# Kernel optimization log

Measured on AMD Instinct MI355X. Metric: run time of the kernel, lower is better.

## Reference

```python
import jax, jax.numpy as jnp
import numpy as np

IMG_SIZE = 640.0
CONF_THRESH = 0.001
NMS_THRESH = 0.6
TOP_K = 1000  # fixed-shape candidate cap per class


def _pairwise_iou(b):
    # b: [K,4] in x1,y1,x2,y2; replicates the numpy NMS math (1e-28 / 1e-14 eps)
    x1, y1, x2, y2 = b[:, 0], b[:, 1], b[:, 2], b[:, 3]
    areas = (x2 - x1) * (y2 - y1)
    xx1 = jnp.maximum(x1[:, None], x1[None, :])
    yy1 = jnp.maximum(y1[:, None], y1[None, :])
    xx2 = jnp.minimum(x2[:, None], x2[None, :])
    yy2 = jnp.minimum(y2[:, None], y2[None, :])
    w = jnp.maximum(1e-28, xx2 - xx1)
    h = jnp.maximum(1e-28, yy2 - yy1)
    inter = w * h
    return inter / (areas[:, None] + areas[None, :] - inter + 1e-14)


def setup_inputs() -> dict:
    key = jax.random.key(0)
    k1, k2, k3 = jax.random.split(key, 3)
    img_size, strides, KA, C = 640, [8, 16, 32], 3, 80
    anchor = np.array([[10, 13], [16, 30], [33, 23], [30, 61], [62, 45], [59, 119],
                       [116, 90], [156, 198], [373, 326]], np.float32).reshape(3, 3, 2)
    grids, anchs, strs = [], [], []
    for lvl, s in enumerate(strides):
        f = img_size // s
        gy, gx = np.meshgrid(np.arange(f), np.arange(f), indexing='ij')
        gxy = np.stack([gx, gy], -1).reshape(-1, 1, 2).astype(np.float32)
        grids.append(np.broadcast_to(gxy, (f * f, KA, 2)).reshape(-1, 2))
        anchs.append(np.broadcast_to(anchor[lvl][None], (f * f, KA, 2)).reshape(-1, 2).astype(np.float32))
        strs.append(np.full((f * f * KA, 1), s, np.float32))
    grid_xy = jnp.asarray(np.concatenate(grids, 0))      # [N,2]
    anchors_wh = jnp.asarray(np.concatenate(anchs, 0))   # [N,2]
    stride_t = jnp.asarray(np.concatenate(strs, 0))      # [N,1]
    N = grid_xy.shape[0]  # 25200
    return {
        'reg_pred': jax.random.normal(k1, (N, 4), jnp.float32),
        'obj_pred': jax.random.normal(k2, (N, 1), jnp.float32),
        'cls_pred': jax.random.normal(k3, (N, C), jnp.float32),
        'grid_xy': grid_xy,
        'anchors_wh': anchors_wh,
        'stride_t': stride_t,
    }


def reference(reg_pred, obj_pred, cls_pred, grid_xy, anchors_wh, stride_t):
    # ---- box decode (YOLO head) ----
    xy = (jax.nn.sigmoid(reg_pred[:, :2]) + grid_xy) * stride_t       # centers in pixels
    wh = jnp.exp(reg_pred[:, 2:]) * anchors_wh                        # sizes in pixels
    boxes = jnp.concatenate([xy - 0.5 * wh, xy + 0.5 * wh], axis=-1)  # [N,4]
    boxes = jnp.clip(boxes / IMG_SIZE, 0.0, 1.0)
    # ---- scoring: sigmoid(obj) * softmax(cls) ----
    scores_all = jax.nn.sigmoid(obj_pred) * jax.nn.softmax(cls_pred, axis=-1)  # [N,C]
    cls_inds = jnp.argmax(scores_all, axis=-1)          # [N]
    scores = jnp.max(scores_all, axis=-1)               # [N]
    C = cls_pred.shape[-1]
    K = TOP_K
    ar = jnp.arange(K)

    def nms_class(c):
        s_c = jnp.where((cls_inds == c) & (scores >= CONF_THRESH), scores, -1.0)
        vals, idx = jax.lax.top_k(s_c, K)               # sorted desc, fixed shape
        b = boxes[idx]                                  # [K,4]
        valid = vals > 0.0
        iou = _pairwise_iou(b)                          # [K,K]

        def body(i, keep):
            sup = keep[i] & (iou[i] > NMS_THRESH) & (ar > i)
            return keep & ~sup

        keep = jax.lax.fori_loop(0, K, body, valid)
        return b, vals, keep

    boxes_out, scores_out, keep = jax.vmap(nms_class)(jnp.arange(C))  # [C,K,4],[C,K],[C,K]
    return boxes_out, scores_out * keep.astype(scores_out.dtype), keep
```

## Files before the change

kernel.cpp:

```cpp
#include <hip/hip_runtime.h>
#include <cstdint>
#include <cstddef>

#define N_CLS 80
#define TOPK 1000
#define POOL_N 2048
#define MCAP 512
#define BD 1024
#define DTB 128
#define NBLK 197
#define SLICE 32
#define LDSB_STRIDE 10

__global__ __launch_bounds__(DTB) void decode_kernel(
    const float* __restrict__ reg, const float* __restrict__ obj,
    const float* __restrict__ cls, const float* __restrict__ grid,
    const float* __restrict__ anch, const float* __restrict__ strd,
    float* __restrict__ boxes, uint2* __restrict__ scs,
    int* __restrict__ cnts, uint2* __restrict__ gpool2, int N) {
  __shared__ int hcnt[N_CLS];
  __shared__ uint2 lpool[N_CLS * SLICE];
  const int blk = blockIdx.x;
  const int tid = threadIdx.x;
  const int i = blk * DTB + tid;

  if (tid < N_CLS) hcnt[tid] = 0;
  __syncthreads();

  const bool valid = (i < N);
  float best = -1.0f;
  int bc = 0;

  if (valid) {
    const float4 r = ((const float4*)reg)[i];
    const float2 g = ((const float2*)grid)[i];
    const float2 aw = ((const float2*)anch)[i];
    const float st = strd[i];

    float cx = (1.0f / (1.0f + expf(-r.x)) + g.x) * st;
    float cy = (1.0f / (1.0f + expf(-r.y)) + g.y) * st;
    float w = expf(r.z) * aw.x;
    float h = expf(r.w) * aw.y;
    float b0 = fminf(fmaxf((cx - 0.5f * w) / 640.0f, 0.0f), 1.0f);
    float b1 = fminf(fmaxf((cy - 0.5f * h) / 640.0f, 0.0f), 1.0f);
    float b2 = fminf(fmaxf((cx + 0.5f * w) / 640.0f, 0.0f), 1.0f);
    float b3 = fminf(fmaxf((cy + 0.5f * h) / 640.0f, 0.0f), 1.0f);
    float4 bo; bo.x = b0; bo.y = b1; bo.z = b2; bo.w = b3;
    ((float4*)boxes)[i] = bo;

    const float4* cr = (const float4*)cls + (size_t)i * 20;

    float mx;
    {
      float4 v = cr[0];
      mx = v.x;
      mx = fmaxf(mx, v.y); mx = fmaxf(mx, v.z); mx = fmaxf(mx, v.w);
#pragma unroll
      for (int q = 1; q < 20; ++q) {
        float4 u = cr[q];
        mx = fmaxf(mx, u.x); mx = fmaxf(mx, u.y);
        mx = fmaxf(mx, u.z); mx = fmaxf(mx, u.w);
      }
    }
    asm volatile("" ::: "memory");

    float s = 0.0f;
#pragma unroll
    for (int q = 0; q < 20; ++q) {
      float4 u = cr[q];
      s += expf(u.x - mx); s += expf(u.y - mx);
      s += expf(u.z - mx); s += expf(u.w - mx);
    }
    asm volatile("" ::: "memory");

    float sig = 1.0f / (1.0f + expf(-obj[i]));

#pragma unroll
    for (int q = 0; q < 20; ++q) {
      float4 u = cr[q];
      float e0 = expf(u.x - mx), e1 = expf(u.y - mx);
      float e2 = expf(u.z - mx), e3 = expf(u.w - mx);
      float q0 = sig * (e0 / s);
      if (q0 > best) { best = q0; bc = 4 * q + 0; }
      float q1 = sig * (e1 / s);
      if (q1 > best) { best = q1; bc = 4 * q + 1; }
      float q2 = sig * (e2 / s);
      if (q2 > best) { best = q2; bc = 4 * q + 2; }
      float q3 = sig * (e3 / s);
      if (q3 > best) { best = q3; bc = 4 * q + 3; }
    }
    scs[i] = make_uint2(__float_as_uint(best), (unsigned)bc);
  }

  const bool pos = valid && (best >= 0.001f);
  if (pos) {
    int slot = atomicAdd(&hcnt[bc], 1);
    if (slot < SLICE)
      lpool[bc * SLICE + slot] = make_uint2(__float_as_uint(best), (unsigned)i);
  }
  __syncthreads();
  if (tid < N_CLS) cnts[blk * N_CLS + tid] = min(hcnt[tid], SLICE);
  for (int t = tid; t < N_CLS * SLICE; t += DTB) {
    int c = t / SLICE, sl = t - c * SLICE;
    gpool2[((size_t)c * NBLK + blk) * SLICE + sl] = lpool[t];
  }
}

__device__ __forceinline__ unsigned long long kinit(int w, int m) {
  int lo = w << 6;
  return (m <= lo) ? 0ULL : ((m - lo >= 64) ? ~0ULL : ((1ULL << (m - lo)) - 1ULL));
}

__global__ __launch_bounds__(BD) void nms_kernel(
    const float* __restrict__ boxes, const uint2* __restrict__ scs,
    const int* __restrict__ cnts, const uint2* __restrict__ gpool2,
    float* __restrict__ out, int N) {
  const int c = blockIdx.x;
  const int tid = threadIdx.x;

  __shared__ uint2 pool[POOL_N];
  __shared__ float svals[TOPK];
  __shared__ int sidx[TOPK];
  __shared__ __align__(16) float4 bxyz[TOPK];
  __shared__ __align__(16) unsigned long long ldsB[MCAP * LDSB_STRIDE];
  __shared__ unsigned char kp[TOPK];
  __shared__ __align__(16) unsigned long long kmbuf[2][8];
  __shared__ int wsum[BD / 64 + 1];
  __shared__ int pref[NBLK + 1];

  if (tid < 64) {
    int carry = 0;
    if (tid == 0) pref[0] = 0;
    for (int ch = 0; ch < (NBLK + 63) / 64; ++ch) {
      int b = ch * 64 + tid;
      int v = (b < NBLK) ? cnts[b * N_CLS + c] : 0;
#pragma unroll
      for (int s = 1; s < 64; s <<= 1) {
        int u = __shfl_up(v, s, 64);
        if (tid >= (unsigned)s) v += u;
      }
      if (b < NBLK) pref[b + 1] = min(carry + v, POOL_N);
      carry += __shfl(v, 63, 64);
    }
  }
  __syncthreads();
  const int cnt = pref[NBLK];
  const int m = min(cnt, TOPK);

  const uint2* gp = gpool2 + (size_t)c * NBLK * SLICE;
  for (int t = tid; t < cnt; t += BD) {
    int lo = 0, hi = NBLK;
    while (hi - lo > 1) {
      int mid = (lo + hi) >> 1;
      if (t >= pref[mid]) lo = mid; else hi = mid;
    }
    pool[t] = gp[(size_t)lo * SLICE + (t - pref[lo])];
  }
  __syncthreads();

  for (int e = tid; e < cnt; e += BD) {
    uint2 me = pool[e];
    float v = __uint_as_float(me.x);
    int idx = (int)me.y;
    int r = 0;
#pragma unroll 8
    for (int k = 0; k < cnt; ++k) {
      uint2 q = pool[k];
      float vk = __uint_as_float(q.x);
      r += (int)((vk > v) || (vk == v && (int)q.y < idx));
    }
    if (r < TOPK) { svals[r] = v; sidx[r] = idx; }
  }
  __syncthreads();

  const int M = TOPK - m;
  if (M > 0) {
    int i = tid;
    bool f = false;
    if (i < N) {
      uint2 sc = scs[i];
      f = !((int)sc.y == c && __uint_as_float(sc.x) >= 0.001f);
    }
    unsigned long long mk = __ballot(f ? 1 : 0);
    int lane = tid & 63, wv = tid >> 6;
    int pre = __popcll(mk & ((1ULL << lane) - 1ULL));
    if (lane == 0) wsum[wv] = __popcll(mk);
    __syncthreads();
    if (tid == 0) {
      int acc = 0;
      for (int wq = 0; wq < BD / 64; ++wq) { int t2 = wsum[wq]; wsum[wq] = acc; acc += t2; }
    }
    __syncthreads();
    int pos = wsum[wv] + pre;
    if (f && pos < M) sidx[m + pos] = i;
  }
  __syncthreads();

  const float4* bf4 = (const float4*)boxes;
  for (int t = tid; t < TOPK; t += BD) bxyz[t] = bf4[sidx[t]];
  __syncthreads();

  const int W = (m + 63) >> 6;
  const bool fast = (m > 0) && (m <= MCAP);
  int cur = 0;

  if (fast) {
    const int tasks = m * W;
    for (int q = tid; q < tasks; q += BD) {
      int w = q / m;
      int j = q - w * m;
      unsigned long long bits = 0ULL;
      if (w <= (j >> 6)) {
        float4 jb = bxyz[j];
        float aj = (jb.z - jb.x) * (jb.w - jb.y);
        int i0 = w << 6, iend = min(i0 + 64, j);
        for (int i = i0; i < iend; ++i) {
          float4 ib = bxyz[i];
          float ai = (ib.z - ib.x) * (ib.w - ib.y);
          float xx1 = fmaxf(ib.x, jb.x), yy1 = fmaxf(ib.y, jb.y);
          float xx2 = fminf(ib.z, jb.z), yy2 = fminf(ib.w, jb.w);
          float ww = fmaxf(1e-28f, xx2 - xx1), hh = fmaxf(1e-28f, yy2 - yy1);
          float inter = ww * hh;
          float iou = inter / (ai + aj - inter + 1e-14f);
          if (iou > 0.6f) bits |= (1ULL << (i - i0));
        }
      }
      ldsB[(size_t)j * LDSB_STRIDE + w] = bits;
    }
    __syncthreads();

    ulonglong2 ta, tb, tc, td;
    ta = tb = tc = td = make_ulonglong2(0ULL, 0ULL);
    if (tid < m) {
      const ulonglong2* rp = (const ulonglong2*)&ldsB[(size_t)tid * LDSB_STRIDE];
      ta = rp[0]; tb = rp[1]; tc = rp[2]; td = rp[3];
    }
    if (tid < 8) kmbuf[0][tid] = kinit(tid, m);
    __syncthreads();

    for (;;) {
      bool keep = false;
      if (tid < m) {
        unsigned long long sup =
            (ta.x & kmbuf[cur][0]) | (ta.y & kmbuf[cur][1]) |
            (tb.x & kmbuf[cur][2]) | (tb.y & kmbuf[cur][3]) |
            (tc.x & kmbuf[cur][4]) | (tc.y & kmbuf[cur][5]) |
            (td.x & kmbuf[cur][6]) | (td.y & kmbuf[cur][7]);
        keep = (sup == 0ULL);
      }
      bool old = (tid < m) &&
                 ((kmbuf[cur][tid >> 6] >> (tid & 63)) & 1ULL);
      unsigned long long bl = __ballot(keep ? 1 : 0);
      int wv = tid >> 6;
      if ((tid & 63) == 0 && wv < 8) kmbuf[cur ^ 1][wv] = bl;
      int any = __syncthreads_or((int)(keep != old));
      cur ^= 1;
      if (!any) break;
    }
  } else {
    for (int t = tid; t < TOPK; t += BD) kp[t] = (t < m) ? 1 : 0;
    __syncthreads();
    for (int i = 0; i < m; ++i) {
      if (kp[i]) {
        float4 rb = bxyz[i];
        float ai = (rb.z - rb.x) * (rb.w - rb.y);
        for (int j = i + 1 + tid; j < m; j += BD) {
          if (kp[j]) {
            float4 jb = bxyz[j];
            float aj = (jb.z - jb.x) * (jb.w - jb.y);
            float xx1 = fmaxf(rb.x, jb.x), yy1 = fmaxf(rb.y, jb.y);
            float xx2 = fminf(rb.z, jb.z), yy2 = fminf(rb.w, jb.w);
            float ww = fmaxf(1e-28f, xx2 - xx1), hh = fmaxf(1e-28f, yy2 - yy1);
            float inter = ww * hh;
            float iou = inter / (ai + aj - inter + 1e-14f);
            if (iou > 0.6f) kp[j] = 0;
          }
        }
      }
      __syncthreads();
    }
  }

  float* outB = out;
  float* outS = out + N_CLS * TOPK * 4;
  float* outK = outS + N_CLS * TOPK;
  for (int t = tid; t < TOPK; t += BD) {
    float k = 0.0f;
    if (t < m)
      k = fast ? (float)((kmbuf[cur][t >> 6] >> (t & 63)) & 1ULL)
               : (float)kp[t];
    float v = (t < m) ? svals[t] : -1.0f;
    ((float4*)outB)[c * TOPK + t] = bxyz[t];
    outS[c * TOPK + t] = v * k;
    outK[c * TOPK + t] = k;
  }
}

extern "C" void kernel_launch(void* const* d_in, const int* in_sizes, int n_in,
                              void* d_out, int out_size, void* d_ws, size_t ws_size,
                              hipStream_t stream) {
  const float* reg  = (const float*)d_in[0];
  const float* obj  = (const float*)d_in[1];
  const float* cls  = (const float*)d_in[2];
  const float* grid = (const float*)d_in[3];
  const float* anch = (const float*)d_in[4];
  const float* strd = (const float*)d_in[5];
  const int N = in_sizes[0] / 4;

  char* w8 = (char*)d_ws;
  size_t off = 0;
  float* boxes  = (float*)(w8 + off); off += (size_t)N * 16;
  uint2* scs    = (uint2*)(w8 + off); off += (size_t)N * 8;
  int*   cnts   = (int*)(w8 + off);   off += (size_t)NBLK * N_CLS * 4;
  uint2* gpool2 = (uint2*)(w8 + off); off += (size_t)N_CLS * NBLK * SLICE * 8;
  float* out = (float*)d_out;

  decode_kernel<<<NBLK, DTB, 0, stream>>>(
      reg, obj, cls, grid, anch, strd, boxes, scs, cnts, gpool2, N);
  nms_kernel<<<N_CLS, BD, 0, stream>>>(boxes, scs, cnts, gpool2, out, N);
}
```

Baseline: 117.4 us.

## Decode boxes lazily in NMS kernel and drop full-size box/score buffers

```diff
diff --git a/kernel.cpp b/kernel.cpp
--- a/kernel.cpp
+++ b/kernel.cpp
@@ -13,13 +13,9 @@
 #define LDSB_STRIDE 10
 
 __global__ __launch_bounds__(DTB) void decode_kernel(
-    const float* __restrict__ reg, const float* __restrict__ obj,
-    const float* __restrict__ cls, const float* __restrict__ grid,
-    const float* __restrict__ anch, const float* __restrict__ strd,
-    float* __restrict__ boxes, uint2* __restrict__ scs,
+    const float* __restrict__ obj, const float* __restrict__ cls,
     int* __restrict__ cnts, uint2* __restrict__ gpool2, int N) {
   __shared__ int hcnt[N_CLS];
-  __shared__ uint2 lpool[N_CLS * SLICE];
   const int blk = blockIdx.x;
   const int tid = threadIdx.x;
   const int i = blk * DTB + tid;
@@ -32,22 +28,6 @@
   int bc = 0;
 
   if (valid) {
-    const float4 r = ((const float4*)reg)[i];
-    const float2 g = ((const float2*)grid)[i];
-    const float2 aw = ((const float2*)anch)[i];
-    const float st = strd[i];
-
-    float cx = (1.0f / (1.0f + expf(-r.x)) + g.x) * st;
-    float cy = (1.0f / (1.0f + expf(-r.y)) + g.y) * st;
-    float w = expf(r.z) * aw.x;
-    float h = expf(r.w) * aw.y;
-    float b0 = fminf(fmaxf((cx - 0.5f * w) / 640.0f, 0.0f), 1.0f);
-    float b1 = fminf(fmaxf((cy - 0.5f * h) / 640.0f, 0.0f), 1.0f);
-    float b2 = fminf(fmaxf((cx + 0.5f * w) / 640.0f, 0.0f), 1.0f);
-    float b3 = fminf(fmaxf((cy + 0.5f * h) / 640.0f, 0.0f), 1.0f);
-    float4 bo; bo.x = b0; bo.y = b1; bo.z = b2; bo.w = b3;
-    ((float4*)boxes)[i] = bo;
-
     const float4* cr = (const float4*)cls + (size_t)i * 20;
 
     float mx;
@@ -89,21 +69,16 @@
       float q3 = sig * (e3 / s);
       if (q3 > best) { best = q3; bc = 4 * q + 3; }
     }
-    scs[i] = make_uint2(__float_as_uint(best), (unsigned)bc);
   }
 
   const bool pos = valid && (best >= 0.001f);
-  if (pos) {
-    int slot = atomicAdd(&hcnt[bc], 1);
-    if (slot < SLICE)
-      lpool[bc * SLICE + slot] = make_uint2(__float_as_uint(best), (unsigned)i);
-  }
-  __syncthreads();
-  if (tid < N_CLS) cnts[blk * N_CLS + tid] = min(hcnt[tid], SLICE);
-  for (int t = tid; t < N_CLS * SLICE; t += DTB) {
-    int c = t / SLICE, sl = t - c * SLICE;
-    gpool2[((size_t)c * NBLK + blk) * SLICE + sl] = lpool[t];
-  }
+  int slot = -1;
+  if (pos) slot = atomicAdd(&hcnt[bc], 1);
+  __syncthreads();
+  if (tid < N_CLS) cnts[tid * NBLK + blk] = min(hcnt[tid], SLICE);
+  if (pos && slot < SLICE)
+    gpool2[((size_t)bc * NBLK + blk) * SLICE + slot] =
+        make_uint2(__float_as_uint(best), (unsigned)i);
 }
 
 __device__ __forceinline__ unsigned long long kinit(int w, int m) {
@@ -112,7 +87,8 @@
 }
 
 __global__ __launch_bounds__(BD) void nms_kernel(
-    const float* __restrict__ boxes, const uint2* __restrict__ scs,
+    const float* __restrict__ reg, const float* __restrict__ grid,
+    const float* __restrict__ anch, const float* __restrict__ strd,
     const int* __restrict__ cnts, const uint2* __restrict__ gpool2,
     float* __restrict__ out, int N) {
   const int c = blockIdx.x;
@@ -127,13 +103,15 @@
   __shared__ __align__(16) unsigned long long kmbuf[2][8];
   __shared__ int wsum[BD / 64 + 1];
   __shared__ int pref[NBLK + 1];
+  __shared__ unsigned fmap[32];
 
   if (tid < 64) {
+    const int* cc = cnts + c * NBLK;
     int carry = 0;
     if (tid == 0) pref[0] = 0;
     for (int ch = 0; ch < (NBLK + 63) / 64; ++ch) {
       int b = ch * 64 + tid;
-      int v = (b < NBLK) ? cnts[b * N_CLS + c] : 0;
+      int v = (b < NBLK) ? cc[b] : 0;
 #pragma unroll
       for (int s = 1; s < 64; s <<= 1) {
         int u = __shfl_up(v, s, 64);
@@ -143,6 +121,7 @@
       carry += __shfl(v, 63, 64);
     }
   }
+  if (tid < 32) fmap[tid] = 0u;
   __syncthreads();
   const int cnt = pref[NBLK];
   const int m = min(cnt, TOPK);
@@ -157,6 +136,11 @@
     pool[t] = gp[(size_t)lo * SLICE + (t - pref[lo])];
   }
   __syncthreads();
+
+  for (int t = tid; t < cnt; t += BD) {
+    unsigned idx = pool[t].y;
+    if (idx < 1024u) atomicOr(&fmap[idx >> 5], 1u << (idx & 31u));
+  }
 
   for (int e = tid; e < cnt; e += BD) {
     uint2 me = pool[e];
@@ -175,12 +159,7 @@
 
   const int M = TOPK - m;
   if (M > 0) {
-    int i = tid;
-    bool f = false;
-    if (i < N) {
-      uint2 sc = scs[i];
-      f = !((int)sc.y == c && __uint_as_float(sc.x) >= 0.001f);
-    }
+    bool f = !((fmap[tid >> 5] >> (tid & 31u)) & 1u);
     unsigned long long mk = __ballot(f ? 1 : 0);
     int lane = tid & 63, wv = tid >> 6;
     int pre = __popcll(mk & ((1ULL << lane) - 1ULL));
@@ -192,12 +171,27 @@
     }
     __syncthreads();
     int pos = wsum[wv] + pre;
-    if (f && pos < M) sidx[m + pos] = i;
-  }
-  __syncthreads();
-
-  const float4* bf4 = (const float4*)boxes;
-  for (int t = tid; t < TOPK; t += BD) bxyz[t] = bf4[sidx[t]];
+    if (f && pos < M) sidx[m + pos] = tid;
+  }
+  __syncthreads();
+
+  for (int t = tid; t < TOPK; t += BD) {
+    int idx = sidx[t];
+    const float4 r = ((const float4*)reg)[idx];
+    const float2 g = ((const float2*)grid)[idx];
+    const float2 aw = ((const float2*)anch)[idx];
+    const float st = strd[idx];
+    float cx = (1.0f / (1.0f + expf(-r.x)) + g.x) * st;
+    float cy = (1.0f / (1.0f + expf(-r.y)) + g.y) * st;
+    float w = expf(r.z) * aw.x;
+    float h = expf(r.w) * aw.y;
+    float4 bo;
+    bo.x = fminf(fmaxf((cx - 0.5f * w) / 640.0f, 0.0f), 1.0f);
+    bo.y = fminf(fmaxf((cy - 0.5f * h) / 640.0f, 0.0f), 1.0f);
+    bo.z = fminf(fmaxf((cx + 0.5f * w) / 640.0f, 0.0f), 1.0f);
+    bo.w = fminf(fmaxf((cy + 0.5f * h) / 640.0f, 0.0f), 1.0f);
+    bxyz[t] = bo;
+  }
   __syncthreads();
 
   const int W = (m + 63) >> 6;
@@ -309,13 +303,11 @@
 
   char* w8 = (char*)d_ws;
   size_t off = 0;
-  float* boxes  = (float*)(w8 + off); off += (size_t)N * 16;
-  uint2* scs    = (uint2*)(w8 + off); off += (size_t)N * 8;
-  int*   cnts   = (int*)(w8 + off);   off += (size_t)NBLK * N_CLS * 4;
+  int*   cnts   = (int*)(w8 + off);   off += (size_t)N_CLS * NBLK * 4;
   uint2* gpool2 = (uint2*)(w8 + off); off += (size_t)N_CLS * NBLK * SLICE * 8;
   float* out = (float*)d_out;
 
-  decode_kernel<<<NBLK, DTB, 0, stream>>>(
-      reg, obj, cls, grid, anch, strd, boxes, scs, cnts, gpool2, N);
-  nms_kernel<<<N_CLS, BD, 0, stream>>>(boxes, scs, cnts, gpool2, out, N);
+  decode_kernel<<<NBLK, DTB, 0, stream>>>(obj, cls, cnts, gpool2, N);
+  nms_kernel<<<N_CLS, BD, 0, stream>>>(reg, grid, anch, strd, cnts, gpool2,
+                                       out, N);
 }
```

New measurement: 118.9 us. No clear change (+1.3%).
